# Performance work log

Hardware: AMD Instinct MI355X
Metric: run time of the kernel (lower is better)

The kernel has to match this reference:

```python
import jax, jax.numpy as jnp
import numpy as np

H = 4  # num_heads
EPS = 1e-5


def setup_inputs() -> dict:
    key = jax.random.key(0)
    ks = jax.random.split(key, 12)
    N, C, E = 4096, 128, 131072
    x = jax.random.normal(ks[0], (N, C), dtype=jnp.float32)
    edge_index = jax.random.randint(ks[1], (2, E), 0, N, dtype=jnp.int64)
    # guarantee every row has at least one neighbor (self-loops) to avoid NaN softmax rows
    loops = jnp.arange(N, dtype=jnp.int64)
    edge_index = edge_index.at[0, :N].set(loops).at[1, :N].set(loops)
    s = 1.0 / np.sqrt(C)
    def lin(k):
        kw, kb = jax.random.split(k)
        return (jax.random.uniform(kw, (C, C), jnp.float32, -s, s),
                jax.random.uniform(kb, (C,), jnp.float32, -s, s))
    wq, bq = lin(ks[2]); wk, bk = lin(ks[3]); wv, bv = lin(ks[4]); wo, bo = lin(ks[5])
    gamma = jnp.ones((C,), jnp.float32)
    beta = jnp.zeros((C,), jnp.float32)
    return {"x": x, "edge_index": edge_index, "wq": wq, "bq": bq, "wk": wk, "bk": bk,
            "wv": wv, "bv": bv, "wo": wo, "bo": bo, "gamma": gamma, "beta": beta}


def reference(x, edge_index, wq, bq, wk, bk, wv, bv, wo, bo, gamma, beta):
    N, C = x.shape
    D = C // H
    q = (x @ wq.T + bq).reshape(N, H, D)
    k = (x @ wk.T + bk).reshape(N, H, D)
    v = (x @ wv.T + bv).reshape(N, H, D)
    scores = jnp.einsum('nhd,mhd->nhm', q, k) / jnp.sqrt(jnp.float32(D))  # [N,H,N]
    row, col = edge_index
    mask = jnp.zeros((N, N), jnp.float32).at[row, col].set(1.0)
    scores = jnp.where(mask[:, None, :] == 0, -jnp.inf, scores)
    attn = jax.nn.softmax(scores, axis=-1)  # dropout is identity in eval
    out = jnp.einsum('nhm,mhd->nhd', attn, v).reshape(N, C)
    out = out @ wo.T + bo
    y = x + out
    mu = jnp.mean(y, axis=-1, keepdims=True)
    var = jnp.var(y, axis=-1, keepdims=True)
    return (y - mu) / jnp.sqrt(var + EPS) * gamma + beta
```

## Files before the change

### kernel.cpp

```cpp
#include <hip/hip_runtime.h>

typedef unsigned long long u64;
typedef unsigned int u32;
typedef unsigned short u16;

#define C_DIM 128
#define D_DIM 32
#define MAXN 256

__global__ __launch_bounds__(256) void zero_bm(u64* bm, int nwords) {
    int i = blockIdx.x * 256 + threadIdx.x;
    if (i < nwords) bm[i] = 0ull;
}

__global__ __launch_bounds__(256) void build_bm(const int* __restrict__ row,
                                                const int* __restrict__ col,
                                                int E, int wpr, u64* __restrict__ bm) {
    int e = blockIdx.x * 256 + threadIdx.x;
    if (e < E) {
        int r = row[e];
        int c = col[e];
        atomicOr(&bm[(size_t)r * wpr + (c >> 6)], 1ull << (c & 63));
    }
}

__global__ __launch_bounds__(256, 2) void qkv_kernel(
    const float* __restrict__ x,
    const float* __restrict__ wq, const float* __restrict__ bq,
    const float* __restrict__ wk, const float* __restrict__ bk,
    const float* __restrict__ wv, const float* __restrict__ bv,
    float* __restrict__ qo, float* __restrict__ ko, float* __restrict__ vo)
{
    const int ROWS = 16;
    const int WSTR = C_DIM + 4;
    __shared__ float xs[ROWS][C_DIM];
    __shared__ float wt[C_DIM * WSTR];
    int t = threadIdx.x;
    int n0 = blockIdx.x * ROWS;
    #pragma unroll
    for (int i = 0; i < 2; ++i) {
        int g = t + i * 256;
        int r = g >> 5, c4 = (g & 31) << 2;
        *(float4*)&xs[r][c4] = *(const float4*)(x + (size_t)(n0 + r) * C_DIM + c4);
    }
    int jg = t & 31;
    int r0 = (t >> 5) * 2;
    const float* Wp[3] = {wq, wk, wv};
    const float* Bp[3] = {bq, bk, bv};
    float*       Op[3] = {qo, ko, vo};
    for (int s = 0; s < 3; ++s) {
        __syncthreads();
        const float* W = Wp[s];
        #pragma unroll
        for (int i = 0; i < 16; ++i) {
            int g = t + i * 256;
            int j = g >> 5, c4 = (g & 31) << 2;
            *(float4*)&wt[j * WSTR + c4] = *(const float4*)(W + (size_t)j * C_DIM + c4);
        }
        __syncthreads();
        const float* B = Bp[s];
        float acc[4][2];
        #pragma unroll
        for (int jj = 0; jj < 4; ++jj) {
            float b = B[jg + jj * 32];
            acc[jj][0] = b; acc[jj][1] = b;
        }
        for (int c = 0; c < C_DIM; c += 4) {
            float4 xa = *(const float4*)&xs[r0][c];
            float4 xb = *(const float4*)&xs[r0 + 1][c];
            #pragma unroll
            for (int jj = 0; jj < 4; ++jj) {
                float4 w4 = *(const float4*)&wt[(jg + jj * 32) * WSTR + c];
                acc[jj][0] += w4.x * xa.x + w4.y * xa.y + w4.z * xa.z + w4.w * xa.w;
                acc[jj][1] += w4.x * xb.x + w4.y * xb.y + w4.z * xb.z + w4.w * xb.w;
            }
        }
        float* O = Op[s];
        #pragma unroll
        for (int jj = 0; jj < 4; ++jj) {
            int j = jg + jj * 32;
            O[(size_t)(n0 + r0) * C_DIM + j]     = acc[jj][0];
            O[(size_t)(n0 + r0 + 1) * C_DIM + j] = acc[jj][1];
        }
    }
}

__global__ __launch_bounds__(256) void attn_kernel(
    const float* __restrict__ q, const float* __restrict__ k,
    const float* __restrict__ v, const u16* __restrict__ bm16,
    float* __restrict__ out, int chunks_per_row)
{
    int n = blockIdx.x;
    int t = threadIdx.x;
    __shared__ float qs[C_DIM];
    __shared__ int lm[MAXN];
    __shared__ float ls[4][MAXN];
    __shared__ float po[2][C_DIM];
    __shared__ float sminv[4];
    __shared__ int cnt;
    if (t == 0) cnt = 0;
    if (t < C_DIM) qs[t] = q[(size_t)n * C_DIM + t];
    __syncthreads();
    u32 w = (t < chunks_per_row) ? (u32)bm16[(size_t)n * chunks_per_row + t] : 0u;
    while (w) {
        int b = __ffs(w) - 1;
        w &= w - 1;
        int idx = atomicAdd(&cnt, 1);
        if (idx < MAXN) lm[idx] = t * 16 + b;
    }
    __syncthreads();
    int c = cnt < MAXN ? cnt : MAXN;
    int wave = t >> 6, lane = t & 63;
    const float scale = 0.17677669529663687f;
    for (int jj = wave; jj < c; jj += 4) {
        const float* kr = k + (size_t)lm[jj] * C_DIM;
        float p0 = qs[lane] * kr[lane];
        float p1 = qs[64 + lane] * kr[64 + lane];
        #pragma unroll
        for (int off = 16; off; off >>= 1) {
            p0 += __shfl_xor(p0, off);
            p1 += __shfl_xor(p1, off);
        }
        if (lane == 0)       { ls[0][jj] = p0 * scale; ls[2][jj] = p1 * scale; }
        else if (lane == 32) { ls[1][jj] = p0 * scale; ls[3][jj] = p1 * scale; }
    }
    __syncthreads();
    {
        int h = wave;
        float mx = -1e30f;
        for (int jj = lane; jj < c; jj += 64) mx = fmaxf(mx, ls[h][jj]);
        #pragma unroll
        for (int off = 32; off; off >>= 1) mx = fmaxf(mx, __shfl_xor(mx, off));
        float sum = 0.f;
        for (int jj = lane; jj < c; jj += 64) {
            float e = __expf(ls[h][jj] - mx);
            ls[h][jj] = e;
            sum += e;
        }
        #pragma unroll
        for (int off = 32; off; off >>= 1) sum += __shfl_xor(sum, off);
        if (lane == 0) sminv[h] = 1.0f / sum;
    }
    __syncthreads();
    {
        int d = t & 127, part = t >> 7, h = d >> 5;
        float acc = 0.f;
        for (int jj = part; jj < c; jj += 2)
            acc += ls[h][jj] * v[(size_t)lm[jj] * C_DIM + d];
        po[part][d] = acc;
    }
    __syncthreads();
    if (t < C_DIM)
        out[(size_t)n * C_DIM + t] = (po[0][t] + po[1][t]) * sminv[t >> 5];
}

__global__ __launch_bounds__(256, 2) void oproj_ln_kernel(
    const float* __restrict__ ao, const float* __restrict__ wo, const float* __restrict__ bo,
    const float* __restrict__ x, const float* __restrict__ gamma, const float* __restrict__ beta,
    float* __restrict__ out)
{
    const int ROWS = 16;
    const int WSTR = C_DIM + 4;
    __shared__ float xs[ROWS][C_DIM];
    __shared__ float wt[C_DIM * WSTR];
    int t = threadIdx.x;
    int n0 = blockIdx.x * ROWS;
    #pragma unroll
    for (int i = 0; i < 2; ++i) {
        int g = t + i * 256;
        int r = g >> 5, c4 = (g & 31) << 2;
        *(float4*)&xs[r][c4] = *(const float4*)(ao + (size_t)(n0 + r) * C_DIM + c4);
    }
    #pragma unroll
    for (int i = 0; i < 16; ++i) {
        int g = t + i * 256;
        int j = g >> 5, c4 = (g & 31) << 2;
        *(float4*)&wt[j * WSTR + c4] = *(const float4*)(wo + (size_t)j * C_DIM + c4);
    }
    __syncthreads();
    int jg = t & 31, r0 = (t >> 5) * 2;
    float acc[4][2];
    #pragma unroll
    for (int jj = 0; jj < 4; ++jj) {
        float b = bo[jg + jj * 32];
        acc[jj][0] = b; acc[jj][1] = b;
    }
    for (int c = 0; c < C_DIM; c += 4) {
        float4 xa = *(const float4*)&xs[r0][c];
        float4 xb = *(const float4*)&xs[r0 + 1][c];
        #pragma unroll
        for (int jj = 0; jj < 4; ++jj) {
            float4 w4 = *(const float4*)&wt[(jg + jj * 32) * WSTR + c];
            acc[jj][0] += w4.x * xa.x + w4.y * xa.y + w4.z * xa.z + w4.w * xa.w;
            acc[jj][1] += w4.x * xb.x + w4.y * xb.y + w4.z * xb.z + w4.w * xb.w;
        }
    }
    __syncthreads();
    #pragma unroll
    for (int jj = 0; jj < 4; ++jj) {
        int j = jg + jj * 32;
        xs[r0][j]     = acc[jj][0] + x[(size_t)(n0 + r0) * C_DIM + j];
        xs[r0 + 1][j] = acc[jj][1] + x[(size_t)(n0 + r0 + 1) * C_DIM + j];
    }
    __syncthreads();
    int wave = t >> 6, lane = t & 63;
    #pragma unroll
    for (int rr = 0; rr < 4; ++rr) {
        int r = wave * 4 + rr;
        float y0 = xs[r][lane], y1 = xs[r][64 + lane];
        float s = y0 + y1, s2 = y0 * y0 + y1 * y1;
        #pragma unroll
        for (int off = 32; off; off >>= 1) {
            s  += __shfl_xor(s, off);
            s2 += __shfl_xor(s2, off);
        }
        float mu = s * (1.0f / 128.0f);
        float var = s2 * (1.0f / 128.0f) - mu * mu;
        float rstd = rsqrtf(var + 1e-5f);
        size_t o = (size_t)(n0 + r) * C_DIM;
        out[o + lane]      = (y0 - mu) * rstd * gamma[lane] + beta[lane];
        out[o + 64 + lane] = (y1 - mu) * rstd * gamma[64 + lane] + beta[64 + lane];
    }
}

extern "C" void kernel_launch(void* const* d_in, const int* in_sizes, int n_in,
                              void* d_out, int out_size, void* d_ws, size_t ws_size,
                              hipStream_t stream)
{
    const float* x     = (const float*)d_in[0];
    const int*   ei    = (const int*)d_in[1];
    const float* wq    = (const float*)d_in[2];
    const float* bq    = (const float*)d_in[3];
    const float* wk    = (const float*)d_in[4];
    const float* bk    = (const float*)d_in[5];
    const float* wv    = (const float*)d_in[6];
    const float* bv    = (const float*)d_in[7];
    const float* wo    = (const float*)d_in[8];
    const float* bo    = (const float*)d_in[9];
    const float* gamma = (const float*)d_in[10];
    const float* beta  = (const float*)d_in[11];
    float* out = (float*)d_out;

    int N = in_sizes[0] / C_DIM;
    int E = in_sizes[1] / 2;
    int wpr = N >> 6;
    int cpr = N >> 4;

    size_t mat_bytes = (size_t)N * C_DIM * sizeof(float);
    char* base = (char*)d_ws;
    float* q  = (float*)(base);
    float* k  = (float*)(base + mat_bytes);
    float* v  = (float*)(base + 2 * mat_bytes);
    float* ao = (float*)(base + 3 * mat_bytes);
    u64*   bm = (u64*)(base + 4 * mat_bytes);

    int nwords = N * wpr;
    zero_bm<<<(nwords + 255) / 256, 256, 0, stream>>>(bm, nwords);
    build_bm<<<(E + 255) / 256, 256, 0, stream>>>(ei, ei + E, E, wpr, bm);
    qkv_kernel<<<N / 16, 256, 0, stream>>>(x, wq, bq, wk, bk, wv, bv, q, k, v);
    attn_kernel<<<N, 256, 0, stream>>>(q, k, v, (const u16*)bm, ao, cpr);
    oproj_ln_kernel<<<N / 16, 256, 0, stream>>>(ao, wo, bo, x, gamma, beta, out);
}
```

Before: 144.3 us.

## Fuse bitmap build into QKV kernel and attention into out-proj+LayerNorm kernel

Merges the edge-bitmap construction into the QKV projection kernel through a grid-stride loop, and replaces the separate zero kernel with hipMemsetAsync. Attention moves into the output-projection/LayerNorm kernel: each wave processes 4 rows, builds neighbour lists with a popcount prefix scan, batches K/V gathers 8 at a time, and writes results straight to shared memory. This removes two launches and the round trip of the attention output through global memory. In exchange the attention grid shrinks from N blocks to N/16, which lowers parallelism, and MAXN drops to 128, so rows with more neighbours are truncated.

```diff
diff --git a/kernel.cpp b/kernel.cpp
--- a/kernel.cpp
+++ b/kernel.cpp
@@ -5,26 +5,10 @@
 typedef unsigned short u16;
 
 #define C_DIM 128
-#define D_DIM 32
-#define MAXN 256
-
-__global__ __launch_bounds__(256) void zero_bm(u64* bm, int nwords) {
-    int i = blockIdx.x * 256 + threadIdx.x;
-    if (i < nwords) bm[i] = 0ull;
-}
-
-__global__ __launch_bounds__(256) void build_bm(const int* __restrict__ row,
-                                                const int* __restrict__ col,
-                                                int E, int wpr, u64* __restrict__ bm) {
-    int e = blockIdx.x * 256 + threadIdx.x;
-    if (e < E) {
-        int r = row[e];
-        int c = col[e];
-        atomicOr(&bm[(size_t)r * wpr + (c >> 6)], 1ull << (c & 63));
-    }
-}
-
-__global__ __launch_bounds__(256, 2) void qkv_kernel(
+#define MAXN 128
+
+__global__ __launch_bounds__(256) void build_qkv_kernel(
+    const int* __restrict__ ei, int E, u64* __restrict__ bm, int wpr,
     const float* __restrict__ x,
     const float* __restrict__ wq, const float* __restrict__ bq,
     const float* __restrict__ wk, const float* __restrict__ bk,
@@ -37,6 +21,14 @@
     __shared__ float wt[C_DIM * WSTR];
     int t = threadIdx.x;
     int n0 = blockIdx.x * ROWS;
+
+    int stride = gridDim.x * 256;
+    for (int e = blockIdx.x * 256 + t; e < E; e += stride) {
+        int r = ei[e];
+        int c = ei[E + e];
+        atomicOr(&bm[(size_t)r * wpr + (c >> 6)], 1ull << (c & 63));
+    }
+
     #pragma unroll
     for (int i = 0; i < 2; ++i) {
         int g = t + i * 256;
@@ -85,99 +77,125 @@
     }
 }
 
-__global__ __launch_bounds__(256) void attn_kernel(
+__global__ __launch_bounds__(256) void attn_oln_kernel(
     const float* __restrict__ q, const float* __restrict__ k,
-    const float* __restrict__ v, const u16* __restrict__ bm16,
-    float* __restrict__ out, int chunks_per_row)
-{
-    int n = blockIdx.x;
-    int t = threadIdx.x;
-    __shared__ float qs[C_DIM];
-    __shared__ int lm[MAXN];
-    __shared__ float ls[4][MAXN];
-    __shared__ float po[2][C_DIM];
-    __shared__ float sminv[4];
-    __shared__ int cnt;
-    if (t == 0) cnt = 0;
-    if (t < C_DIM) qs[t] = q[(size_t)n * C_DIM + t];
-    __syncthreads();
-    u32 w = (t < chunks_per_row) ? (u32)bm16[(size_t)n * chunks_per_row + t] : 0u;
-    while (w) {
-        int b = __ffs(w) - 1;
-        w &= w - 1;
-        int idx = atomicAdd(&cnt, 1);
-        if (idx < MAXN) lm[idx] = t * 16 + b;
-    }
-    __syncthreads();
-    int c = cnt < MAXN ? cnt : MAXN;
-    int wave = t >> 6, lane = t & 63;
-    const float scale = 0.17677669529663687f;
-    for (int jj = wave; jj < c; jj += 4) {
-        const float* kr = k + (size_t)lm[jj] * C_DIM;
-        float p0 = qs[lane] * kr[lane];
-        float p1 = qs[64 + lane] * kr[64 + lane];
-        #pragma unroll
-        for (int off = 16; off; off >>= 1) {
-            p0 += __shfl_xor(p0, off);
-            p1 += __shfl_xor(p1, off);
-        }
-        if (lane == 0)       { ls[0][jj] = p0 * scale; ls[2][jj] = p1 * scale; }
-        else if (lane == 32) { ls[1][jj] = p0 * scale; ls[3][jj] = p1 * scale; }
-    }
-    __syncthreads();
-    {
-        int h = wave;
-        float mx = -1e30f;
-        for (int jj = lane; jj < c; jj += 64) mx = fmaxf(mx, ls[h][jj]);
-        #pragma unroll
-        for (int off = 32; off; off >>= 1) mx = fmaxf(mx, __shfl_xor(mx, off));
-        float sum = 0.f;
-        for (int jj = lane; jj < c; jj += 64) {
-            float e = __expf(ls[h][jj] - mx);
-            ls[h][jj] = e;
-            sum += e;
-        }
-        #pragma unroll
-        for (int off = 32; off; off >>= 1) sum += __shfl_xor(sum, off);
-        if (lane == 0) sminv[h] = 1.0f / sum;
-    }
-    __syncthreads();
-    {
-        int d = t & 127, part = t >> 7, h = d >> 5;
-        float acc = 0.f;
-        for (int jj = part; jj < c; jj += 2)
-            acc += ls[h][jj] * v[(size_t)lm[jj] * C_DIM + d];
-        po[part][d] = acc;
-    }
-    __syncthreads();
-    if (t < C_DIM)
-        out[(size_t)n * C_DIM + t] = (po[0][t] + po[1][t]) * sminv[t >> 5];
-}
-
-__global__ __launch_bounds__(256, 2) void oproj_ln_kernel(
-    const float* __restrict__ ao, const float* __restrict__ wo, const float* __restrict__ bo,
-    const float* __restrict__ x, const float* __restrict__ gamma, const float* __restrict__ beta,
+    const float* __restrict__ v, const u64* __restrict__ bm, int wpr,
+    const float* __restrict__ x,
+    const float* __restrict__ wo, const float* __restrict__ bo,
+    const float* __restrict__ gamma, const float* __restrict__ beta,
     float* __restrict__ out)
 {
     const int ROWS = 16;
     const int WSTR = C_DIM + 4;
+    __shared__ float wt[C_DIM * WSTR];
     __shared__ float xs[ROWS][C_DIM];
-    __shared__ float wt[C_DIM * WSTR];
+    __shared__ int   lm[4][MAXN];
+    __shared__ float ls[4][4][MAXN];
     int t = threadIdx.x;
     int n0 = blockIdx.x * ROWS;
-    #pragma unroll
-    for (int i = 0; i < 2; ++i) {
-        int g = t + i * 256;
-        int r = g >> 5, c4 = (g & 31) << 2;
-        *(float4*)&xs[r][c4] = *(const float4*)(ao + (size_t)(n0 + r) * C_DIM + c4);
-    }
+    int wave = t >> 6, lane = t & 63;
+
     #pragma unroll
     for (int i = 0; i < 16; ++i) {
         int g = t + i * 256;
         int j = g >> 5, c4 = (g & 31) << 2;
         *(float4*)&wt[j * WSTR + c4] = *(const float4*)(wo + (size_t)j * C_DIM + c4);
     }
-    __syncthreads();
+
+    const float scale = 0.17677669529663687f;
+    for (int it = 0; it < 4; ++it) {
+        int rl = wave + it * 4;
+        int n = n0 + rl;
+        float q0 = q[(size_t)n * C_DIM + lane];
+        float q1 = q[(size_t)n * C_DIM + 64 + lane];
+        u64 bits = bm[(size_t)n * wpr + lane];
+        int pc = __popcll(bits);
+        int incl = pc;
+        #pragma unroll
+        for (int off = 1; off < 64; off <<= 1) {
+            int tv = __shfl_up(incl, off);
+            if (lane >= off) incl += tv;
+        }
+        int cnt = __shfl(incl, 63);
+        int pos = incl - pc;
+        u64 bb = bits;
+        while (bb) {
+            int b = __builtin_ctzll(bb);
+            bb &= bb - 1;
+            if (pos < MAXN) lm[wave][pos] = (lane << 6) + b;
+            ++pos;
+        }
+        if (cnt > MAXN) cnt = MAXN;
+        __syncthreads();
+        for (int j0 = 0; j0 < cnt; j0 += 8) {
+            int cc = cnt - j0; if (cc > 8) cc = 8;
+            float k0a[8], k1a[8];
+            #pragma unroll
+            for (int u = 0; u < 8; ++u) {
+                if (u < cc) {
+                    int m = lm[wave][j0 + u];
+                    k0a[u] = k[(size_t)m * C_DIM + lane];
+                    k1a[u] = k[(size_t)m * C_DIM + 64 + lane];
+                }
+            }
+            #pragma unroll
+            for (int u = 0; u < 8; ++u) {
+                if (u < cc) {
+                    float p0 = q0 * k0a[u];
+                    float p1 = q1 * k1a[u];
+                    #pragma unroll
+                    for (int off = 16; off; off >>= 1) {
+                        p0 += __shfl_xor(p0, off);
+                        p1 += __shfl_xor(p1, off);
+                    }
+                    int jj = j0 + u;
+                    if (lane == 0)       { ls[wave][0][jj] = p0 * scale; ls[wave][2][jj] = p1 * scale; }
+                    else if (lane == 32) { ls[wave][1][jj] = p0 * scale; ls[wave][3][jj] = p1 * scale; }
+                }
+            }
+        }
+        __syncthreads();
+        int g = lane >> 4, li = lane & 15;
+        float mx = -1e30f;
+        for (int jj = li; jj < cnt; jj += 16) mx = fmaxf(mx, ls[wave][g][jj]);
+        #pragma unroll
+        for (int off = 8; off; off >>= 1) mx = fmaxf(mx, __shfl_xor(mx, off));
+        float sum = 0.f;
+        for (int jj = li; jj < cnt; jj += 16) {
+            float e = __expf(ls[wave][g][jj] - mx);
+            ls[wave][g][jj] = e;
+            sum += e;
+        }
+        #pragma unroll
+        for (int off = 8; off; off >>= 1) sum += __shfl_xor(sum, off);
+        float sinv = 1.0f / sum;
+        __syncthreads();
+        int h0 = lane >> 5;
+        float s0 = __shfl(sinv, h0 * 16);
+        float s1 = __shfl(sinv, (h0 + 2) * 16);
+        float a0 = 0.f, a1 = 0.f;
+        for (int j0 = 0; j0 < cnt; j0 += 8) {
+            int cc = cnt - j0; if (cc > 8) cc = 8;
+            float v0a[8], v1a[8], w0a[8], w1a[8];
+            #pragma unroll
+            for (int u = 0; u < 8; ++u) {
+                if (u < cc) {
+                    int m = lm[wave][j0 + u];
+                    v0a[u] = v[(size_t)m * C_DIM + lane];
+                    v1a[u] = v[(size_t)m * C_DIM + 64 + lane];
+                    w0a[u] = ls[wave][h0][j0 + u];
+                    w1a[u] = ls[wave][h0 + 2][j0 + u];
+                }
+            }
+            #pragma unroll
+            for (int u = 0; u < 8; ++u) {
+                if (u < cc) { a0 += w0a[u] * v0a[u]; a1 += w1a[u] * v1a[u]; }
+            }
+        }
+        xs[rl][lane]      = a0 * s0;
+        xs[rl][64 + lane] = a1 * s1;
+        __syncthreads();
+    }
     int jg = t & 31, r0 = (t >> 5) * 2;
     float acc[4][2];
     #pragma unroll
@@ -203,7 +221,6 @@
         xs[r0 + 1][j] = acc[jj][1] + x[(size_t)(n0 + r0 + 1) * C_DIM + j];
     }
     __syncthreads();
-    int wave = t >> 6, lane = t & 63;
     #pragma unroll
     for (int rr = 0; rr < 4; ++rr) {
         int r = wave * 4 + rr;
@@ -244,20 +261,17 @@
     int N = in_sizes[0] / C_DIM;
     int E = in_sizes[1] / 2;
     int wpr = N >> 6;
-    int cpr = N >> 4;
 
     size_t mat_bytes = (size_t)N * C_DIM * sizeof(float);
     char* base = (char*)d_ws;
     float* q  = (float*)(base);
     float* k  = (float*)(base + mat_bytes);
     float* v  = (float*)(base + 2 * mat_bytes);
-    float* ao = (float*)(base + 3 * mat_bytes);
-    u64*   bm = (u64*)(base + 4 * mat_bytes);
-
-    int nwords = N * wpr;
-    zero_bm<<<(nwords + 255) / 256, 256, 0, stream>>>(bm, nwords);
-    build_bm<<<(E + 255) / 256, 256, 0, stream>>>(ei, ei + E, E, wpr, bm);
-    qkv_kernel<<<N / 16, 256, 0, stream>>>(x, wq, bq, wk, bk, wv, bv, q, k, v);
-    attn_kernel<<<N, 256, 0, stream>>>(q, k, v, (const u16*)bm, ao, cpr);
-    oproj_ln_kernel<<<N / 16, 256, 0, stream>>>(ao, wo, bo, x, gamma, beta, out);
+    u64*   bm = (u64*)(base + 3 * mat_bytes);
+
+    hipMemsetAsync(bm, 0, (size_t)N * wpr * sizeof(u64), stream);
+    build_qkv_kernel<<<N / 16, 256, 0, stream>>>(ei, E, bm, wpr,
+                                                 x, wq, bq, wk, bk, wv, bv, q, k, v);
+    attn_oln_kernel<<<N / 16, 256, 0, stream>>>(q, k, v, bm, wpr,
+                                                x, wo, bo, gamma, beta, out);
 }
```

Result: slower. 205.7 us (+42.5%).
